# Optimization experiments

Hardware: AMD Instinct MI355X
Metric: run time of the kernel (lower is better)

The kernel has to match this reference:

```python
import jax, jax.numpy as jnp
import numpy as np


def _squash(t):
    # squash along axis=2 (the atoms axis of [B, D, A, 1, 1])
    norm = jnp.linalg.norm(t, axis=2, keepdims=True)
    n2 = norm * norm
    return t / norm * (n2 / (1.0 + n2))


def setup_inputs() -> dict:
    key = jax.random.key(0)
    k1, k2 = jax.random.split(key)
    B, I, Ain, D, A = 32, 2048, 16, 32, 16
    x = jax.random.normal(k1, (B, I, Ain, 1, 1), jnp.float32)
    weights = 0.1 * jax.random.normal(k2, (I, Ain, D * A, 1, 1), jnp.float32)
    bias = jnp.full((D, A, 1, 1), 0.1, jnp.float32)  # nn.init.constant_(0.1)
    return {"x": x, "weights": weights, "bias": bias, "num_routing": 3}


def reference(x, weights, bias, num_routing):
    B, I, Ain = x.shape[:3]
    D, A = bias.shape[:2]
    # Vote computation (standard voting): sum over input_atoms.
    # Torch does expand+mul+sum; einsum is the same math without the 4.8GB intermediate.
    votes = jnp.einsum('bia,iao->bio', x[:, :, :, 0, 0],
                       weights[:, :, :, 0, 0]).reshape(B, I, D, A, 1, 1)
    votes_sg = jax.lax.stop_gradient(votes)  # votes_trans_stopped in torch
    logits = jnp.zeros((B, I, D, 1, 1), x.dtype)
    activation = None
    for i in range(num_routing):
        route = jax.nn.softmax(logits, axis=2)  # [B, I, D, 1, 1], softmax over D
        v = votes if i == num_routing - 1 else votes_sg
        # route broadcast over atoms axis; sum over input capsules I
        preact = jnp.sum(route[:, :, :, None] * v, axis=1) + bias  # [B, D, A, 1, 1]
        activation = _squash(preact)
        if i < num_routing - 1:
            # agreement update uses non-stopped votes (as in torch)
            logits = logits + jnp.sum(votes * activation[:, None], axis=3)  # [B, I, D, 1, 1]
    return activation
```

## Files before the change

kernel.cpp:

```cpp
#include <hip/hip_runtime.h>


#define B_  32
#define I_  2048
#define K_  16
#define O_  512
#define NG_ 256
#define IC_ 8

template<int PASS>
__global__ __launch_bounds__(256)
void sweep_kernel(const float* __restrict__ x, const float* __restrict__ W,
                  const float* __restrict__ act0_g, const float* __restrict__ act1_g,
                  float* __restrict__ partial)
{
    const int tid  = threadIdx.x;
    const int lane = tid & 63;
    const int wave = tid >> 6;
    const int ig   = blockIdx.x >> 1;
    const int bh   = blockIdx.x & 1;
    const int d    = lane >> 1;
    const int h    = lane & 1;
    const int obase = d * 16 + h * 8;

    const int wv   = __builtin_amdgcn_readfirstlane(wave);
    const int bbase = bh * 16 + wv * 4;

    __shared__ float sW[K_ * O_];

    float facc[4][8];
    #pragma unroll
    for (int bb = 0; bb < 4; ++bb)
        #pragma unroll
        for (int j = 0; j < 8; ++j) facc[bb][j] = 0.f;

    float a0[4][8], a1[4][8];
    if (PASS >= 1) {
        #pragma unroll
        for (int bb = 0; bb < 4; ++bb) {
            const float4* p = (const float4*)(act0_g + (bbase + bb) * O_ + obase);
            float4 f0 = p[0], f1 = p[1];
            a0[bb][0]=f0.x; a0[bb][1]=f0.y; a0[bb][2]=f0.z; a0[bb][3]=f0.w;
            a0[bb][4]=f1.x; a0[bb][5]=f1.y; a0[bb][6]=f1.z; a0[bb][7]=f1.w;
        }
    }
    if (PASS == 2) {
        #pragma unroll
        for (int bb = 0; bb < 4; ++bb) {
            const float4* p = (const float4*)(act1_g + (bbase + bb) * O_ + obase);
            float4 f0 = p[0], f1 = p[1];
            a1[bb][0]=f0.x; a1[bb][1]=f0.y; a1[bb][2]=f0.z; a1[bb][3]=f0.w;
            a1[bb][4]=f1.x; a1[bb][5]=f1.y; a1[bb][6]=f1.z; a1[bb][7]=f1.w;
        }
    }

    for (int ii = 0; ii < IC_; ++ii) {
        const int i = ig * IC_ + ii;
        __syncthreads();
        {
            const float4* Wg = (const float4*)(W + (size_t)i * (K_ * O_));
            #pragma unroll
            for (int q = 0; q < 8; ++q) {
                const int f  = tid + 256 * q;
                float4 w4 = Wg[f];
                const int e0 = 4 * f;
                const int k  = e0 >> 9;
                const int o  = e0 & (O_ - 1);
                const int dd = o >> 4;
                const int aa = o & 15;
                const int hh = aa >> 3;
                const int jq = (aa >> 2) & 1;
                *(float4*)&sW[jq * 4096 + k * 256 + (dd * 2 + hh) * 4] = w4;
            }
        }
        float xs[4][16];
        #pragma unroll
        for (int bb = 0; bb < 4; ++bb) {
            const float4* xp = (const float4*)(x + ((size_t)(bbase + bb) * I_ + i) * K_);
            #pragma unroll
            for (int q = 0; q < 4; ++q) {
                float4 v = xp[q];
                xs[bb][4*q+0]=v.x; xs[bb][4*q+1]=v.y; xs[bb][4*q+2]=v.z; xs[bb][4*q+3]=v.w;
            }
        }
        __syncthreads();

        float V[4][8];
        #pragma unroll
        for (int bb = 0; bb < 4; ++bb)
            #pragma unroll
            for (int j = 0; j < 8; ++j) V[bb][j] = 0.f;
        #pragma unroll
        for (int k = 0; k < K_; ++k) {
            const float4 w0 = *(const float4*)&sW[k * 256 + lane * 4];
            const float4 w1 = *(const float4*)&sW[4096 + k * 256 + lane * 4];
            const float w[8] = {w0.x, w0.y, w0.z, w0.w, w1.x, w1.y, w1.z, w1.w};
            #pragma unroll
            for (int bb = 0; bb < 4; ++bb) {
                const float xb = xs[bb][k];
                #pragma unroll
                for (int j = 0; j < 8; ++j) V[bb][j] = fmaf(xb, w[j], V[bb][j]);
            }
        }

        #pragma unroll
        for (int bb = 0; bb < 4; ++bb) {
            if (PASS == 0) {
                #pragma unroll
                for (int j = 0; j < 8; ++j) facc[bb][j] += V[bb][j];
            } else {
                float p0 = 0.f;
                #pragma unroll
                for (int j = 0; j < 8; ++j) p0 = fmaf(V[bb][j], a0[bb][j], p0);
                p0 += __shfl_xor(p0, 1);
                float lg = p0;
                if (PASS == 2) {
                    float p1 = 0.f;
                    #pragma unroll
                    for (int j = 0; j < 8; ++j) p1 = fmaf(V[bb][j], a1[bb][j], p1);
                    p1 += __shfl_xor(p1, 1);
                    lg += p1;
                }
                const float e = __expf(lg);
                float s = e;
                s += __shfl_xor(s, 2);
                s += __shfl_xor(s, 4);
                s += __shfl_xor(s, 8);
                s += __shfl_xor(s, 16);
                s += __shfl_xor(s, 32);
                const float r = e * __builtin_amdgcn_rcpf(s);
                #pragma unroll
                for (int j = 0; j < 8; ++j)
                    facc[bb][j] = fmaf(r, V[bb][j], facc[bb][j]);
            }
        }
    }

    #pragma unroll
    for (int bb = 0; bb < 4; ++bb) {
        const int b = bbase + bb;
        float4* dst = (float4*)(partial + ((size_t)ig * B_ + b) * O_ + obase);
        dst[0] = make_float4(facc[bb][0], facc[bb][1], facc[bb][2], facc[bb][3]);
        dst[1] = make_float4(facc[bb][4], facc[bb][5], facc[bb][6], facc[bb][7]);
    }
}

__global__ __launch_bounds__(256)
void reduce_squash(const float* __restrict__ partial, const float* __restrict__ bias,
                   float scale, float* __restrict__ out)
{
    const int t  = threadIdx.x;
    const int g  = blockIdx.x * 32 + (t & 31);
    const int sl = t >> 5;
    float s = 0.f;
    #pragma unroll
    for (int w = sl * 32; w < sl * 32 + 32; ++w)
        s += partial[(size_t)w * (B_ * O_) + g];
    __shared__ float red[256];
    red[t] = s;
    __syncthreads();
    if (t < 32) {
        float v = red[t];
        #pragma unroll
        for (int r = 1; r < 8; ++r) v += red[t + 32 * r];
        const float p = fmaf(v, scale, bias[g & (O_ - 1)]);
        float nn = p * p;
        nn += __shfl_xor(nn, 1);
        nn += __shfl_xor(nn, 2);
        nn += __shfl_xor(nn, 4);
        nn += __shfl_xor(nn, 8);
        out[g] = p * sqrtf(nn) / (1.f + nn);
    }
}

extern "C" void kernel_launch(void* const* d_in, const int* in_sizes, int n_in,
                              void* d_out, int out_size, void* d_ws, size_t ws_size,
                              hipStream_t stream) {
    const float* x    = (const float*)d_in[0];
    const float* W    = (const float*)d_in[1];
    const float* bias = (const float*)d_in[2];
    float* out = (float*)d_out;

    float* partial = (float*)d_ws;
    float* act0    = partial + (size_t)NG_ * B_ * O_;
    float* act1    = act0 + B_ * O_;

    sweep_kernel<0><<<NG_ * 2, 256, 0, stream>>>(x, W, nullptr, nullptr, partial);
    reduce_squash<<<512, 256, 0, stream>>>(partial, bias, 1.f / 32.f, act0);
    sweep_kernel<1><<<NG_ * 2, 256, 0, stream>>>(x, W, act0, nullptr, partial);
    reduce_squash<<<512, 256, 0, stream>>>(partial, bias, 1.f, act1);
    sweep_kernel<2><<<NG_ * 2, 256, 0, stream>>>(x, W, act0, act1, partial);
    reduce_squash<<<512, 256, 0, stream>>>(partial, bias, 1.f, out);
}
```

Baseline: 188.4 us.

## Cover all batches per block, stream weights straight into LDS, merge activations

Each sweep block now has 512 threads covering all 32 batches for 4 input capsules. Each weight slice is therefore fetched from global memory once instead of by two half-batch blocks. Weights are copied into LDS with global_load_lds in their natural layout, which drops the register staging and the scatter remap. The two routing agreement dot products are folded into one by summing act0 and act1 up front, removing a shuffle and a dot product per batch. The reduce kernel now uses float4 loads over twice as many partial slices. Risks are lower occupancy from larger blocks, 2-way LDS bank conflicts on the strided float4 reads, and more partial-sum traffic.

```diff
diff --git a/kernel.cpp b/kernel.cpp
--- a/kernel.cpp
+++ b/kernel.cpp
@@ -5,11 +5,14 @@
 #define I_  2048
 #define K_  16
 #define O_  512
-#define NG_ 256
-#define IC_ 8
+#define NG_ 512
+#define IC_ 4
+
+typedef const __attribute__((address_space(1))) uint32_t* gp_t;
+typedef __attribute__((address_space(3))) uint32_t* lp_t;
 
 template<int PASS>
-__global__ __launch_bounds__(256)
+__global__ __launch_bounds__(512, 4)
 void sweep_kernel(const float* __restrict__ x, const float* __restrict__ W,
                   const float* __restrict__ act0_g, const float* __restrict__ act1_g,
                   float* __restrict__ partial)
@@ -17,14 +20,11 @@
     const int tid  = threadIdx.x;
     const int lane = tid & 63;
     const int wave = tid >> 6;
-    const int ig   = blockIdx.x >> 1;
-    const int bh   = blockIdx.x & 1;
-    const int d    = lane >> 1;
-    const int h    = lane & 1;
-    const int obase = d * 16 + h * 8;
+    const int ig   = blockIdx.x;
+    const int obase = lane * 8;
 
-    const int wv   = __builtin_amdgcn_readfirstlane(wave);
-    const int bbase = bh * 16 + wv * 4;
+    const int wv    = __builtin_amdgcn_readfirstlane(wave);
+    const int bbase = wv * 4;
 
     __shared__ float sW[K_ * O_];
 
@@ -34,23 +34,20 @@
         #pragma unroll
         for (int j = 0; j < 8; ++j) facc[bb][j] = 0.f;
 
-    float a0[4][8], a1[4][8];
+    float as[4][8];
     if (PASS >= 1) {
         #pragma unroll
         for (int bb = 0; bb < 4; ++bb) {
-            const float4* p = (const float4*)(act0_g + (bbase + bb) * O_ + obase);
-            float4 f0 = p[0], f1 = p[1];
-            a0[bb][0]=f0.x; a0[bb][1]=f0.y; a0[bb][2]=f0.z; a0[bb][3]=f0.w;
-            a0[bb][4]=f1.x; a0[bb][5]=f1.y; a0[bb][6]=f1.z; a0[bb][7]=f1.w;
-        }
-    }
-    if (PASS == 2) {
-        #pragma unroll
-        for (int bb = 0; bb < 4; ++bb) {
-            const float4* p = (const float4*)(act1_g + (bbase + bb) * O_ + obase);
-            float4 f0 = p[0], f1 = p[1];
-            a1[bb][0]=f0.x; a1[bb][1]=f0.y; a1[bb][2]=f0.z; a1[bb][3]=f0.w;
-            a1[bb][4]=f1.x; a1[bb][5]=f1.y; a1[bb][6]=f1.z; a1[bb][7]=f1.w;
+            const float4* p0 = (const float4*)(act0_g + (bbase + bb) * O_ + obase);
+            float4 f0 = p0[0], f1 = p0[1];
+            as[bb][0]=f0.x; as[bb][1]=f0.y; as[bb][2]=f0.z; as[bb][3]=f0.w;
+            as[bb][4]=f1.x; as[bb][5]=f1.y; as[bb][6]=f1.z; as[bb][7]=f1.w;
+            if (PASS == 2) {
+                const float4* p1 = (const float4*)(act1_g + (bbase + bb) * O_ + obase);
+                float4 g0 = p1[0], g1 = p1[1];
+                as[bb][0]+=g0.x; as[bb][1]+=g0.y; as[bb][2]+=g0.z; as[bb][3]+=g0.w;
+                as[bb][4]+=g1.x; as[bb][5]+=g1.y; as[bb][6]+=g1.z; as[bb][7]+=g1.w;
+            }
         }
     }
 
@@ -58,19 +55,13 @@
         const int i = ig * IC_ + ii;
         __syncthreads();
         {
-            const float4* Wg = (const float4*)(W + (size_t)i * (K_ * O_));
+            const float* gsrc = W + (size_t)i * (K_ * O_);
             #pragma unroll
-            for (int q = 0; q < 8; ++q) {
-                const int f  = tid + 256 * q;
-                float4 w4 = Wg[f];
-                const int e0 = 4 * f;
-                const int k  = e0 >> 9;
-                const int o  = e0 & (O_ - 1);
-                const int dd = o >> 4;
-                const int aa = o & 15;
-                const int hh = aa >> 3;
-                const int jq = (aa >> 2) & 1;
-                *(float4*)&sW[jq * 4096 + k * 256 + (dd * 2 + hh) * 4] = w4;
+            for (int q = 0; q < 4; ++q) {
+                const int fb = (wave * 4 + q) * 64;
+                __builtin_amdgcn_global_load_lds(
+                    (gp_t)(gsrc + 4 * (fb + lane)),
+                    (lp_t)(&sW[4 * fb]), 16, 0, 0);
             }
         }
         float xs[4][16];
@@ -92,8 +83,8 @@
             for (int j = 0; j < 8; ++j) V[bb][j] = 0.f;
         #pragma unroll
         for (int k = 0; k < K_; ++k) {
-            const float4 w0 = *(const float4*)&sW[k * 256 + lane * 4];
-            const float4 w1 = *(const float4*)&sW[4096 + k * 256 + lane * 4];
+            const float4 w0 = *(const float4*)&sW[k * O_ + obase];
+            const float4 w1 = *(const float4*)&sW[k * O_ + obase + 4];
             const float w[8] = {w0.x, w0.y, w0.z, w0.w, w1.x, w1.y, w1.z, w1.w};
             #pragma unroll
             for (int bb = 0; bb < 4; ++bb) {
@@ -109,18 +100,10 @@
                 #pragma unroll
                 for (int j = 0; j < 8; ++j) facc[bb][j] += V[bb][j];
             } else {
-                float p0 = 0.f;
+                float lg = 0.f;
                 #pragma unroll
-                for (int j = 0; j < 8; ++j) p0 = fmaf(V[bb][j], a0[bb][j], p0);
-                p0 += __shfl_xor(p0, 1);
-                float lg = p0;
-                if (PASS == 2) {
-                    float p1 = 0.f;
-                    #pragma unroll
-                    for (int j = 0; j < 8; ++j) p1 = fmaf(V[bb][j], a1[bb][j], p1);
-                    p1 += __shfl_xor(p1, 1);
-                    lg += p1;
-                }
+                for (int j = 0; j < 8; ++j) lg = fmaf(V[bb][j], as[bb][j], lg);
+                lg += __shfl_xor(lg, 1);
                 const float e = __expf(lg);
                 float s = e;
                 s += __shfl_xor(s, 2);
@@ -149,27 +132,33 @@
 void reduce_squash(const float* __restrict__ partial, const float* __restrict__ bias,
                    float scale, float* __restrict__ out)
 {
-    const int t  = threadIdx.x;
-    const int g  = blockIdx.x * 32 + (t & 31);
-    const int sl = t >> 5;
-    float s = 0.f;
-    #pragma unroll
-    for (int w = sl * 32; w < sl * 32 + 32; ++w)
-        s += partial[(size_t)w * (B_ * O_) + g];
-    __shared__ float red[256];
-    red[t] = s;
+    const int t     = threadIdx.x;
+    const int quad  = t & 15;
+    const int slice = t >> 4;
+    const int gbase = blockIdx.x * 64;
+    const float4* src = (const float4*)partial + (gbase >> 2) + quad;
+
+    float4 acc = make_float4(0.f, 0.f, 0.f, 0.f);
+    #pragma unroll 8
+    for (int w = slice * 32; w < slice * 32 + 32; ++w) {
+        float4 v = src[(size_t)w * (B_ * O_ / 4)];
+        acc.x += v.x; acc.y += v.y; acc.z += v.z; acc.w += v.w;
+    }
+    __shared__ float4 red[256];
+    red[t] = acc;
     __syncthreads();
-    if (t < 32) {
-        float v = red[t];
+    if (t < 64) {
+        float s = 0.f;
         #pragma unroll
-        for (int r = 1; r < 8; ++r) v += red[t + 32 * r];
-        const float p = fmaf(v, scale, bias[g & (O_ - 1)]);
+        for (int sl = 0; sl < 16; ++sl)
+            s += ((const float*)&red[sl * 16 + (t >> 2)])[t & 3];
+        const float p = fmaf(s, scale, bias[(gbase + t) & (O_ - 1)]);
         float nn = p * p;
         nn += __shfl_xor(nn, 1);
         nn += __shfl_xor(nn, 2);
         nn += __shfl_xor(nn, 4);
         nn += __shfl_xor(nn, 8);
-        out[g] = p * sqrtf(nn) / (1.f + nn);
+        out[gbase + t] = p * sqrtf(nn) / (1.f + nn);
     }
 }
 
@@ -185,10 +174,10 @@
     float* act0    = partial + (size_t)NG_ * B_ * O_;
     float* act1    = act0 + B_ * O_;
 
-    sweep_kernel<0><<<NG_ * 2, 256, 0, stream>>>(x, W, nullptr, nullptr, partial);
-    reduce_squash<<<512, 256, 0, stream>>>(partial, bias, 1.f / 32.f, act0);
-    sweep_kernel<1><<<NG_ * 2, 256, 0, stream>>>(x, W, act0, nullptr, partial);
-    reduce_squash<<<512, 256, 0, stream>>>(partial, bias, 1.f, act1);
-    sweep_kernel<2><<<NG_ * 2, 256, 0, stream>>>(x, W, act0, act1, partial);
-    reduce_squash<<<512, 256, 0, stream>>>(partial, bias, 1.f, out);
+    sweep_kernel<0><<<NG_, 512, 0, stream>>>(x, W, nullptr, nullptr, partial);
+    reduce_squash<<<256, 256, 0, stream>>>(partial, bias, 1.f / 32.f, act0);
+    sweep_kernel<1><<<NG_, 512, 0, stream>>>(x, W, act0, nullptr, partial);
+    reduce_squash<<<256, 256, 0, stream>>>(partial, bias, 1.f, act1);
+    sweep_kernel<2><<<NG_, 512, 0, stream>>>(x, W, act0, act1, partial);
+    reduce_squash<<<256, 256, 0, stream>>>(partial, bias, 1.f, out);
 }
```

Measured after the change: 218.2 us. 15.8% more time.
